# Optimization experiments

Hardware: AMD Instinct MI355X
Metric: run time of the kernel (lower is better)

## Reference

```python
import jax, jax.numpy as jnp
import numpy as np
import math

B, H, S, D = 2, 16, 2048, 64


def setup_inputs() -> dict:
    key = jax.random.key(0)
    kq, kk, kv = jax.random.split(key, 3)
    q = jax.random.normal(kq, (B, H, S, D), dtype=jnp.float32)
    k = jax.random.normal(kk, (B, H, S, D), dtype=jnp.float32)
    v = jax.random.normal(kv, (B, H, S, D), dtype=jnp.float32)
    # causal lower-triangular mask, broadcastable to [B, H, S, S]
    mask = jnp.tril(jnp.ones((S, S), dtype=jnp.int32))[None, None, :, :]
    return {"q": q, "k": k, "v": v, "mask": mask}


def reference(q, k, v, mask):
    d_tensor = q.shape[-1]
    # scores: [B, H, S, S] = q @ k^T / sqrt(d)
    scores = jnp.einsum("bhqd,bhkd->bhqk", q, k) / math.sqrt(d_tensor)
    scores = jnp.where(mask == 0, jnp.float32(-100000.0), scores)
    attn = jax.nn.softmax(scores, axis=-1)
    out = jnp.einsum("bhqk,bhkd->bhqd", attn, v)
    return (out, attn)
```

## Files before the change

### kernel.cpp

```cpp
#include <hip/hip_runtime.h>

#define S_LEN 2048
#define D_DIM 64
#define NBH   32
#define BQ    64
#define SCALE 0.125f
#define KST   72

typedef _Float16 half8 __attribute__((ext_vector_type(8)));
typedef _Float16 half4 __attribute__((ext_vector_type(4)));
typedef float    fx4   __attribute__((ext_vector_type(4)));

__global__ __launch_bounds__(256)
void attn_fused(const float* __restrict__ Q, const float* __restrict__ K,
                const float* __restrict__ V, float* __restrict__ Out,
                float* __restrict__ Attn) {
    const int bh  = blockIdx.x;
    const int qt  = (int)(gridDim.y - 1) - (int)blockIdx.y;
    const int q0  = qt * BQ;
    const int T   = qt + 1;

    const int tid  = threadIdx.x;
    const int lane = tid & 63;
    const int w    = tid >> 6;
    const int ln15 = lane & 15;
    const int quad = lane >> 4;

    __shared__ _Float16 q_s[BQ][KST];
    __shared__ _Float16 k_s[64][KST];
    __shared__ _Float16 v_t[64][KST];
    __shared__ _Float16 p_s[4][16][KST];

    const float* Qb = Q + ((size_t)bh * S_LEN + q0) * D_DIM;
    const float* Kb = K + (size_t)bh * S_LEN * D_DIM;
    const float* Vb = V + (size_t)bh * S_LEN * D_DIM;

    {
        const float4* src = (const float4*)Qb;
        for (int i = tid; i < BQ * 16; i += 256) {
            int r = i >> 4, c4 = i & 15;
            float4 f = src[i];
            half4 h = {(_Float16)f.x, (_Float16)f.y, (_Float16)f.z, (_Float16)f.w};
            *(half4*)&q_s[r][c4 * 4] = h;
        }
    }
    __syncthreads();

    const int mrow = w * 16 + ln15;
    half8 a_q0 = *(const half8*)&q_s[mrow][quad * 8];
    half8 a_q1 = *(const half8*)&q_s[mrow][32 + quad * 8];

    const int qrow0 = q0 + w * 16 + quad * 4;

    float m_r[4] = {-1e30f, -1e30f, -1e30f, -1e30f};
    float l_r[4] = {0.f, 0.f, 0.f, 0.f};

    for (int t = 0; t < T; ++t) {
        __syncthreads();
        const float4* ksrc = (const float4*)(Kb + (size_t)t * 64 * D_DIM);
        for (int i = tid; i < 64 * 16; i += 256) {
            int r = i >> 4, c4 = i & 15;
            float4 f = ksrc[i];
            half4 h = {(_Float16)f.x, (_Float16)f.y, (_Float16)f.z, (_Float16)f.w};
            *(half4*)&k_s[r][c4 * 4] = h;
        }
        __syncthreads();

        fx4 sC[4];
        #pragma unroll
        for (int nt = 0; nt < 4; ++nt) {
            fx4 z = {0.f, 0.f, 0.f, 0.f};
            half8 b0 = *(const half8*)&k_s[nt * 16 + ln15][quad * 8];
            half8 b1 = *(const half8*)&k_s[nt * 16 + ln15][32 + quad * 8];
            z = __builtin_amdgcn_mfma_f32_16x16x32_f16(a_q0, b0, z, 0, 0, 0);
            z = __builtin_amdgcn_mfma_f32_16x16x32_f16(a_q1, b1, z, 0, 0, 0);
            sC[nt] = z;
        }

        const int j0 = t * 64;
        float sv[4][4];
        float tmax[4] = {-1e30f, -1e30f, -1e30f, -1e30f};
        #pragma unroll
        for (int nt = 0; nt < 4; ++nt) {
            int jc = j0 + nt * 16 + ln15;
            #pragma unroll
            for (int r = 0; r < 4; ++r) {
                float x = (jc <= qrow0 + r) ? sC[nt][r] * SCALE : -1e30f;
                sv[nt][r] = x;
                tmax[r] = fmaxf(tmax[r], x);
            }
        }
        #pragma unroll
        for (int r = 0; r < 4; ++r) {
            float v = tmax[r];
            v = fmaxf(v, __shfl_xor(v, 1));
            v = fmaxf(v, __shfl_xor(v, 2));
            v = fmaxf(v, __shfl_xor(v, 4));
            v = fmaxf(v, __shfl_xor(v, 8));
            float mn = fmaxf(m_r[r], v);
            float corr = __expf(m_r[r] - mn);
            float ts = 0.f;
            #pragma unroll
            for (int nt = 0; nt < 4; ++nt) ts += __expf(sv[nt][r] - mn);
            ts += __shfl_xor(ts, 1);
            ts += __shfl_xor(ts, 2);
            ts += __shfl_xor(ts, 4);
            ts += __shfl_xor(ts, 8);
            l_r[r] = l_r[r] * corr + ts;
            m_r[r] = mn;
        }
    }

    float inv_l[4];
    #pragma unroll
    for (int r = 0; r < 4; ++r) inv_l[r] = 1.0f / l_r[r];

    fx4 oacc[4];
    #pragma unroll
    for (int dt = 0; dt < 4; ++dt) oacc[dt] = (fx4){0.f, 0.f, 0.f, 0.f};

    for (int t = 0; t < T; ++t) {
        __syncthreads();
        const float4* ksrc = (const float4*)(Kb + (size_t)t * 64 * D_DIM);
        const float4* vsrc = (const float4*)(Vb + (size_t)t * 64 * D_DIM);
        for (int i = tid; i < 64 * 16; i += 256) {
            int r = i >> 4, c4 = i & 15;
            float4 f = ksrc[i];
            half4 h = {(_Float16)f.x, (_Float16)f.y, (_Float16)f.z, (_Float16)f.w};
            *(half4*)&k_s[r][c4 * 4] = h;
            float4 g = vsrc[i];
            v_t[c4 * 4 + 0][r] = (_Float16)g.x;
            v_t[c4 * 4 + 1][r] = (_Float16)g.y;
            v_t[c4 * 4 + 2][r] = (_Float16)g.z;
            v_t[c4 * 4 + 3][r] = (_Float16)g.w;
        }
        __syncthreads();

        fx4 sC[4];
        #pragma unroll
        for (int nt = 0; nt < 4; ++nt) {
            fx4 z = {0.f, 0.f, 0.f, 0.f};
            half8 b0 = *(const half8*)&k_s[nt * 16 + ln15][quad * 8];
            half8 b1 = *(const half8*)&k_s[nt * 16 + ln15][32 + quad * 8];
            z = __builtin_amdgcn_mfma_f32_16x16x32_f16(a_q0, b0, z, 0, 0, 0);
            z = __builtin_amdgcn_mfma_f32_16x16x32_f16(a_q1, b1, z, 0, 0, 0);
            sC[nt] = z;
        }

        const int j0 = t * 64;
        #pragma unroll
        for (int nt = 0; nt < 4; ++nt) {
            int jc = j0 + nt * 16 + ln15;
            #pragma unroll
            for (int r = 0; r < 4; ++r) {
                float x = (jc <= qrow0 + r) ? sC[nt][r] * SCALE : -1e30f;
                float p = __expf(x - m_r[r]) * inv_l[r];
                size_t aidx = ((size_t)bh * S_LEN + (size_t)(qrow0 + r)) * S_LEN + jc;
                Attn[aidx] = p;
                p_s[w][quad * 4 + r][nt * 16 + ln15] = (_Float16)p;
            }
        }
        __syncthreads();

        half8 a_p0 = *(const half8*)&p_s[w][ln15][quad * 8];
        half8 a_p1 = *(const half8*)&p_s[w][ln15][32 + quad * 8];
        #pragma unroll
        for (int dt = 0; dt < 4; ++dt) {
            half8 bv0 = *(const half8*)&v_t[dt * 16 + ln15][quad * 8];
            half8 bv1 = *(const half8*)&v_t[dt * 16 + ln15][32 + quad * 8];
            oacc[dt] = __builtin_amdgcn_mfma_f32_16x16x32_f16(a_p0, bv0, oacc[dt], 0, 0, 0);
            oacc[dt] = __builtin_amdgcn_mfma_f32_16x16x32_f16(a_p1, bv1, oacc[dt], 0, 0, 0);
        }
    }

    #pragma unroll
    for (int dt = 0; dt < 4; ++dt) {
        #pragma unroll
        for (int r = 0; r < 4; ++r) {
            size_t oidx = ((size_t)bh * S_LEN + (size_t)(qrow0 + r)) * D_DIM + dt * 16 + ln15;
            Out[oidx] = oacc[dt][r];
        }
    }

    {
        const int jend = q0 + BQ;
        const int rowlen4 = (S_LEN - jend) >> 2;
        if (rowlen4 > 0) {
            float4 z = {0.f, 0.f, 0.f, 0.f};
            for (int r = w; r < BQ; r += 4) {
                float4* dst = (float4*)(Attn + ((size_t)bh * S_LEN + (size_t)(q0 + r)) * S_LEN + jend);
                for (int c = lane; c < rowlen4; c += 64) dst[c] = z;
            }
        }
    }
}

extern "C" void kernel_launch(void* const* d_in, const int* in_sizes, int n_in,
                              void* d_out, int out_size, void* d_ws, size_t ws_size,
                              hipStream_t stream) {
    const float* q = (const float*)d_in[0];
    const float* k = (const float*)d_in[1];
    const float* v = (const float*)d_in[2];
    float* out  = (float*)d_out;
    float* attn = out + (size_t)NBH * S_LEN * D_DIM;
    dim3 grid(NBH, S_LEN / BQ);
    attn_fused<<<grid, 256, 0, stream>>>(q, k, v, out, attn);
}
```

Baseline: 747.4 us.

## Load K directly to registers, stage probabilities in fp32 LDS, coalesce nontemporal attn stores

K tiles are now read straight from global memory into MFMA operand registers, which removes the K LDS staging and its barriers. V is transposed with vectorized half4 LDS writes. Probabilities are staged in fp32 shared memory and written out as coalesced 16-float row segments with nontemporal stores, replacing scattered scalar stores to the attention matrix. The softmax scale is folded into Q together with log2(e) so exp2f can be used, and the causal mask is applied only on the diagonal tile. The trade-off is redundant global K loads, since every wave reads the full tile, plus extra LDS traffic for the fp32 P buffer.

```diff
diff --git a/kernel.cpp b/kernel.cpp
--- a/kernel.cpp
+++ b/kernel.cpp
@@ -4,8 +4,9 @@
 #define D_DIM 64
 #define NBH   32
 #define BQ    64
-#define SCALE 0.125f
+#define SCALE2 0.1803368801f
 #define KST   72
+#define PST   68
 
 typedef _Float16 half8 __attribute__((ext_vector_type(8)));
 typedef _Float16 half4 __attribute__((ext_vector_type(4)));
@@ -27,9 +28,8 @@
     const int quad = lane >> 4;
 
     __shared__ _Float16 q_s[BQ][KST];
-    __shared__ _Float16 k_s[64][KST];
     __shared__ _Float16 v_t[64][KST];
-    __shared__ _Float16 p_s[4][16][KST];
+    __shared__ float    p_s[4][16][PST];
 
     const float* Qb = Q + ((size_t)bh * S_LEN + q0) * D_DIM;
     const float* Kb = K + (size_t)bh * S_LEN * D_DIM;
@@ -40,15 +40,16 @@
         for (int i = tid; i < BQ * 16; i += 256) {
             int r = i >> 4, c4 = i & 15;
             float4 f = src[i];
-            half4 h = {(_Float16)f.x, (_Float16)f.y, (_Float16)f.z, (_Float16)f.w};
+            half4 h = {(_Float16)(f.x * SCALE2), (_Float16)(f.y * SCALE2),
+                       (_Float16)(f.z * SCALE2), (_Float16)(f.w * SCALE2)};
             *(half4*)&q_s[r][c4 * 4] = h;
         }
     }
     __syncthreads();
 
     const int mrow = w * 16 + ln15;
-    half8 a_q0 = *(const half8*)&q_s[mrow][quad * 8];
-    half8 a_q1 = *(const half8*)&q_s[mrow][32 + quad * 8];
+    const half8 a_q0 = *(const half8*)&q_s[mrow][quad * 8];
+    const half8 a_q1 = *(const half8*)&q_s[mrow][32 + quad * 8];
 
     const int qrow0 = q0 + w * 16 + quad * 4;
 
@@ -56,38 +57,46 @@
     float l_r[4] = {0.f, 0.f, 0.f, 0.f};
 
     for (int t = 0; t < T; ++t) {
-        __syncthreads();
-        const float4* ksrc = (const float4*)(Kb + (size_t)t * 64 * D_DIM);
-        for (int i = tid; i < 64 * 16; i += 256) {
-            int r = i >> 4, c4 = i & 15;
-            float4 f = ksrc[i];
-            half4 h = {(_Float16)f.x, (_Float16)f.y, (_Float16)f.z, (_Float16)f.w};
-            *(half4*)&k_s[r][c4 * 4] = h;
-        }
-        __syncthreads();
-
         fx4 sC[4];
         #pragma unroll
         for (int nt = 0; nt < 4; ++nt) {
+            const float* kj = Kb + (size_t)(t * 64 + nt * 16 + ln15) * D_DIM + quad * 8;
+            float4 f0 = *(const float4*)(kj + 0);
+            float4 f1 = *(const float4*)(kj + 4);
+            float4 f2 = *(const float4*)(kj + 32);
+            float4 f3 = *(const float4*)(kj + 36);
+            half8 b0 = {(_Float16)f0.x, (_Float16)f0.y, (_Float16)f0.z, (_Float16)f0.w,
+                        (_Float16)f1.x, (_Float16)f1.y, (_Float16)f1.z, (_Float16)f1.w};
+            half8 b1 = {(_Float16)f2.x, (_Float16)f2.y, (_Float16)f2.z, (_Float16)f2.w,
+                        (_Float16)f3.x, (_Float16)f3.y, (_Float16)f3.z, (_Float16)f3.w};
             fx4 z = {0.f, 0.f, 0.f, 0.f};
-            half8 b0 = *(const half8*)&k_s[nt * 16 + ln15][quad * 8];
-            half8 b1 = *(const half8*)&k_s[nt * 16 + ln15][32 + quad * 8];
             z = __builtin_amdgcn_mfma_f32_16x16x32_f16(a_q0, b0, z, 0, 0, 0);
             z = __builtin_amdgcn_mfma_f32_16x16x32_f16(a_q1, b1, z, 0, 0, 0);
             sC[nt] = z;
         }
 
-        const int j0 = t * 64;
         float sv[4][4];
         float tmax[4] = {-1e30f, -1e30f, -1e30f, -1e30f};
-        #pragma unroll
-        for (int nt = 0; nt < 4; ++nt) {
-            int jc = j0 + nt * 16 + ln15;
-            #pragma unroll
-            for (int r = 0; r < 4; ++r) {
-                float x = (jc <= qrow0 + r) ? sC[nt][r] * SCALE : -1e30f;
-                sv[nt][r] = x;
-                tmax[r] = fmaxf(tmax[r], x);
+        if (t < T - 1) {
+            #pragma unroll
+            for (int nt = 0; nt < 4; ++nt)
+                #pragma unroll
+                for (int r = 0; r < 4; ++r) {
+                    float x = sC[nt][r];
+                    sv[nt][r] = x;
+                    tmax[r] = fmaxf(tmax[r], x);
+                }
+        } else {
+            const int j0 = t * 64;
+            #pragma unroll
+            for (int nt = 0; nt < 4; ++nt) {
+                int jc = j0 + nt * 16 + ln15;
+                #pragma unroll
+                for (int r = 0; r < 4; ++r) {
+                    float x = (jc <= qrow0 + r) ? sC[nt][r] : -1e30f;
+                    sv[nt][r] = x;
+                    tmax[r] = fmaxf(tmax[r], x);
+                }
             }
         }
         #pragma unroll
@@ -98,10 +107,10 @@
             v = fmaxf(v, __shfl_xor(v, 4));
             v = fmaxf(v, __shfl_xor(v, 8));
             float mn = fmaxf(m_r[r], v);
-            float corr = __expf(m_r[r] - mn);
+            float corr = exp2f(m_r[r] - mn);
             float ts = 0.f;
             #pragma unroll
-            for (int nt = 0; nt < 4; ++nt) ts += __expf(sv[nt][r] - mn);
+            for (int nt = 0; nt < 4; ++nt) ts += exp2f(sv[nt][r] - mn);
             ts += __shfl_xor(ts, 1);
             ts += __shfl_xor(ts, 2);
             ts += __shfl_xor(ts, 4);
@@ -119,58 +128,100 @@
     #pragma unroll
     for (int dt = 0; dt < 4; ++dt) oacc[dt] = (fx4){0.f, 0.f, 0.f, 0.f};
 
+    const int vc4 = tid >> 4;
+    const int vjg = tid & 15;
+
     for (int t = 0; t < T; ++t) {
-        __syncthreads();
-        const float4* ksrc = (const float4*)(Kb + (size_t)t * 64 * D_DIM);
-        const float4* vsrc = (const float4*)(Vb + (size_t)t * 64 * D_DIM);
-        for (int i = tid; i < 64 * 16; i += 256) {
-            int r = i >> 4, c4 = i & 15;
-            float4 f = ksrc[i];
-            half4 h = {(_Float16)f.x, (_Float16)f.y, (_Float16)f.z, (_Float16)f.w};
-            *(half4*)&k_s[r][c4 * 4] = h;
-            float4 g = vsrc[i];
-            v_t[c4 * 4 + 0][r] = (_Float16)g.x;
-            v_t[c4 * 4 + 1][r] = (_Float16)g.y;
-            v_t[c4 * 4 + 2][r] = (_Float16)g.z;
-            v_t[c4 * 4 + 3][r] = (_Float16)g.w;
-        }
-        __syncthreads();
+        const int j0 = t * 64;
+
+        const float4* vsrc = (const float4*)(Vb + (size_t)j0 * D_DIM);
+        float4 g0 = vsrc[(vjg * 4 + 0) * 16 + vc4];
+        float4 g1 = vsrc[(vjg * 4 + 1) * 16 + vc4];
+        float4 g2 = vsrc[(vjg * 4 + 2) * 16 + vc4];
+        float4 g3 = vsrc[(vjg * 4 + 3) * 16 + vc4];
 
         fx4 sC[4];
         #pragma unroll
         for (int nt = 0; nt < 4; ++nt) {
+            const float* kj = Kb + (size_t)(t * 64 + nt * 16 + ln15) * D_DIM + quad * 8;
+            float4 f0 = *(const float4*)(kj + 0);
+            float4 f1 = *(const float4*)(kj + 4);
+            float4 f2 = *(const float4*)(kj + 32);
+            float4 f3 = *(const float4*)(kj + 36);
+            half8 b0 = {(_Float16)f0.x, (_Float16)f0.y, (_Float16)f0.z, (_Float16)f0.w,
+                        (_Float16)f1.x, (_Float16)f1.y, (_Float16)f1.z, (_Float16)f1.w};
+            half8 b1 = {(_Float16)f2.x, (_Float16)f2.y, (_Float16)f2.z, (_Float16)f2.w,
+                        (_Float16)f3.x, (_Float16)f3.y, (_Float16)f3.z, (_Float16)f3.w};
             fx4 z = {0.f, 0.f, 0.f, 0.f};
-            half8 b0 = *(const half8*)&k_s[nt * 16 + ln15][quad * 8];
-            half8 b1 = *(const half8*)&k_s[nt * 16 + ln15][32 + quad * 8];
             z = __builtin_amdgcn_mfma_f32_16x16x32_f16(a_q0, b0, z, 0, 0, 0);
             z = __builtin_amdgcn_mfma_f32_16x16x32_f16(a_q1, b1, z, 0, 0, 0);
             sC[nt] = z;
         }
 
-        const int j0 = t * 64;
-        #pragma unroll
-        for (int nt = 0; nt < 4; ++nt) {
-            int jc = j0 + nt * 16 + ln15;
-            #pragma unroll
-            for (int r = 0; r < 4; ++r) {
-                float x = (jc <= qrow0 + r) ? sC[nt][r] * SCALE : -1e30f;
-                float p = __expf(x - m_r[r]) * inv_l[r];
-                size_t aidx = ((size_t)bh * S_LEN + (size_t)(qrow0 + r)) * S_LEN + jc;
-                Attn[aidx] = p;
-                p_s[w][quad * 4 + r][nt * 16 + ln15] = (_Float16)p;
+        {
+            half4 h0 = {(_Float16)g0.x, (_Float16)g1.x, (_Float16)g2.x, (_Float16)g3.x};
+            half4 h1 = {(_Float16)g0.y, (_Float16)g1.y, (_Float16)g2.y, (_Float16)g3.y};
+            half4 h2 = {(_Float16)g0.z, (_Float16)g1.z, (_Float16)g2.z, (_Float16)g3.z};
+            half4 h3 = {(_Float16)g0.w, (_Float16)g1.w, (_Float16)g2.w, (_Float16)g3.w};
+            *(half4*)&v_t[vc4 * 4 + 0][vjg * 4] = h0;
+            *(half4*)&v_t[vc4 * 4 + 1][vjg * 4] = h1;
+            *(half4*)&v_t[vc4 * 4 + 2][vjg * 4] = h2;
+            *(half4*)&v_t[vc4 * 4 + 3][vjg * 4] = h3;
+        }
+
+        if (t < T - 1) {
+            #pragma unroll
+            for (int nt = 0; nt < 4; ++nt)
+                #pragma unroll
+                for (int r = 0; r < 4; ++r)
+                    p_s[w][quad * 4 + r][nt * 16 + ln15] = exp2f(sC[nt][r] - m_r[r]) * inv_l[r];
+        } else {
+            #pragma unroll
+            for (int nt = 0; nt < 4; ++nt) {
+                int jc = j0 + nt * 16 + ln15;
+                #pragma unroll
+                for (int r = 0; r < 4; ++r) {
+                    float x = (jc <= qrow0 + r) ? sC[nt][r] : -1e30f;
+                    p_s[w][quad * 4 + r][nt * 16 + ln15] = exp2f(x - m_r[r]) * inv_l[r];
+                }
             }
         }
         __syncthreads();
 
-        half8 a_p0 = *(const half8*)&p_s[w][ln15][quad * 8];
-        half8 a_p1 = *(const half8*)&p_s[w][ln15][32 + quad * 8];
-        #pragma unroll
-        for (int dt = 0; dt < 4; ++dt) {
-            half8 bv0 = *(const half8*)&v_t[dt * 16 + ln15][quad * 8];
-            half8 bv1 = *(const half8*)&v_t[dt * 16 + ln15][32 + quad * 8];
-            oacc[dt] = __builtin_amdgcn_mfma_f32_16x16x32_f16(a_p0, bv0, oacc[dt], 0, 0, 0);
-            oacc[dt] = __builtin_amdgcn_mfma_f32_16x16x32_f16(a_p1, bv1, oacc[dt], 0, 0, 0);
-        }
+        {
+            const int arow = tid >> 2;
+            const int seg  = tid & 3;
+            const float* pr = &p_s[arow >> 4][arow & 15][seg * 16];
+            fx4 o0 = *(const fx4*)(pr + 0);
+            fx4 o1 = *(const fx4*)(pr + 4);
+            fx4 o2 = *(const fx4*)(pr + 8);
+            fx4 o3 = *(const fx4*)(pr + 12);
+            float* dst = Attn + ((size_t)bh * S_LEN + (size_t)(q0 + arow)) * S_LEN + j0 + seg * 16;
+            __builtin_nontemporal_store(o0, (fx4*)(dst + 0));
+            __builtin_nontemporal_store(o1, (fx4*)(dst + 4));
+            __builtin_nontemporal_store(o2, (fx4*)(dst + 8));
+            __builtin_nontemporal_store(o3, (fx4*)(dst + 12));
+        }
+
+        {
+            const float* pw = &p_s[w][ln15][0];
+            fx4 pa = *(const fx4*)(pw + quad * 8);
+            fx4 pb = *(const fx4*)(pw + quad * 8 + 4);
+            fx4 pc = *(const fx4*)(pw + 32 + quad * 8);
+            fx4 pd = *(const fx4*)(pw + 32 + quad * 8 + 4);
+            half8 a_p0 = {(_Float16)pa[0], (_Float16)pa[1], (_Float16)pa[2], (_Float16)pa[3],
+                          (_Float16)pb[0], (_Float16)pb[1], (_Float16)pb[2], (_Float16)pb[3]};
+            half8 a_p1 = {(_Float16)pc[0], (_Float16)pc[1], (_Float16)pc[2], (_Float16)pc[3],
+                          (_Float16)pd[0], (_Float16)pd[1], (_Float16)pd[2], (_Float16)pd[3]};
+            #pragma unroll
+            for (int dt = 0; dt < 4; ++dt) {
+                half8 bv0 = *(const half8*)&v_t[dt * 16 + ln15][quad * 8];
+                half8 bv1 = *(const half8*)&v_t[dt * 16 + ln15][32 + quad * 8];
+                oacc[dt] = __builtin_amdgcn_mfma_f32_16x16x32_f16(a_p0, bv0, oacc[dt], 0, 0, 0);
+                oacc[dt] = __builtin_amdgcn_mfma_f32_16x16x32_f16(a_p1, bv1, oacc[dt], 0, 0, 0);
+            }
+        }
+        __syncthreads();
     }
 
     #pragma unroll
@@ -186,10 +237,10 @@
         const int jend = q0 + BQ;
         const int rowlen4 = (S_LEN - jend) >> 2;
         if (rowlen4 > 0) {
-            float4 z = {0.f, 0.f, 0.f, 0.f};
+            fx4 z = {0.f, 0.f, 0.f, 0.f};
             for (int r = w; r < BQ; r += 4) {
-                float4* dst = (float4*)(Attn + ((size_t)bh * S_LEN + (size_t)(q0 + r)) * S_LEN + jend);
-                for (int c = lane; c < rowlen4; c += 64) dst[c] = z;
+                fx4* dst = (fx4*)(Attn + ((size_t)bh * S_LEN + (size_t)(q0 + r)) * S_LEN + jend);
+                for (int c = lane; c < rowlen4; c += 64) __builtin_nontemporal_store(z, dst + c);
             }
         }
     }
```

New measurement: 1.270 ms. 70.0% more time.
